# Performance work log

Hardware: AMD Instinct MI355X
Metric: run time of the kernel (lower is better)

## Reference

```python
import jax, jax.numpy as jnp
import numpy as np

NPG = 128      # nodes per graph = g(4) * e(32), forced by rearrange + cnn1 channels
G, E32 = 4, 32
ALPHA = 1.0    # GCN2Conv(in_channels, 1) -> alpha = 1
BETA = 1.0     # theta=None -> beta = 1


def _gcn_norm(edge_index, edge_weight, n):
    """PyG gcn_norm: add self-loops (w=1), sym-normalize by degree at dst."""
    src, dst = edge_index[0], edge_index[1]
    loop = jnp.arange(n)
    src = jnp.concatenate([src, loop])
    dst = jnp.concatenate([dst, loop])
    w = jnp.concatenate([edge_weight, jnp.ones((n,), edge_weight.dtype)])
    deg = jax.ops.segment_sum(w, dst, num_segments=n)
    dinv = jnp.where(deg > 0, jax.lax.rsqrt(deg), 0.0)
    norm = dinv[src] * w * dinv[dst]
    return src, dst, norm


def _propagate(x, src, dst, norm, n):
    # gather -> weight -> scatter-add (SpMM)
    return jax.ops.segment_sum(x[src] * norm[:, None], dst, num_segments=n)


def setup_inputs() -> dict:
    key = jax.random.key(0)
    ks = jax.random.split(key, 10)
    N, E, C, H, CH = 65536, 524288, 128, 512, 256
    x = jax.random.normal(ks[0], (N, C), jnp.float32)
    edge_index = jax.random.randint(ks[1], (2, E), 0, N, dtype=jnp.int64)
    edge_attr = jax.random.uniform(ks[2], (E,), jnp.float32)
    w1_gcn2 = jax.random.normal(ks[3], (C, C), jnp.float32) / np.float32(np.sqrt(C))
    w_gcn = jax.random.normal(ks[4], (C, H), jnp.float32) / np.float32(np.sqrt(C))
    b_gcn = jnp.zeros((H,), jnp.float32)
    w_cnn1 = jax.random.normal(ks[5], (H, 4 * H), jnp.float32) / np.float32(np.sqrt(4 * H))
    b_cnn1 = jnp.zeros((H,), jnp.float32)
    w_cnn2 = jax.random.normal(ks[6], (CH, H), jnp.float32) / np.float32(np.sqrt(H))
    b_cnn2 = jnp.zeros((CH,), jnp.float32)
    w_lin = jax.random.normal(ks[7], (32 * CH,), jnp.float32) / np.float32(np.sqrt(32 * CH))
    b_lin = jnp.zeros((), jnp.float32)
    return {"x": x, "edge_attr": edge_attr, "w1_gcn2": w1_gcn2, "w_gcn": w_gcn,
            "b_gcn": b_gcn, "w_cnn1": w_cnn1, "b_cnn1": b_cnn1, "w_cnn2": w_cnn2,
            "b_cnn2": b_cnn2, "w_lin": w_lin, "b_lin": b_lin, "edge_index": edge_index}


def reference(x, edge_attr, w1_gcn2, w_gcn, b_gcn, w_cnn1, b_cnn1, w_cnn2, b_cnn2,
              w_lin, b_lin, edge_index):
    n = x.shape[0]
    bs = n // NPG
    src, dst, norm = _gcn_norm(edge_index, edge_attr, n)

    # GCN2Conv(C, layer=1): h = (1-a)*A_hat x + a*x0; out = (1-b)*h + b*(h @ W1)
    h = _propagate(x, src, dst, norm, n)
    h = h * (1.0 - ALPHA) + ALPHA * x
    h = (1.0 - BETA) * h + BETA * (h @ w1_gcn2)

    # GCNConv(C, H): A_hat (h @ W) + b
    h = _propagate(h @ w_gcn, src, dst, norm, n) + b_gcn
    h = jnp.tanh(h)

    f = h.shape[1]  # hidden_channels
    # '(bs g e) f -> bs (g f) e', e=32, g=4
    h = h.reshape(bs, G, E32, f).transpose(0, 1, 3, 2).reshape(bs, G * f, E32)
    # 1x1 convs == per-position linears over channel dim
    h = jax.nn.relu(jnp.einsum('bce,oc->boe', h, w_cnn1) + b_cnn1[None, :, None])
    h = jax.nn.relu(jnp.einsum('bce,oc->boe', h, w_cnn2) + b_cnn2[None, :, None])
    # dropout p=0.5 is identity in eval mode
    h = h.reshape(bs, -1)
    out = h @ w_lin + b_lin
    return jax.nn.sigmoid(out)
```

## Files before the change

### kernel.cpp

```cpp
#include <hip/hip_runtime.h>
#include <hip/hip_bf16.h>

#define N_NODES 65536
#define N_EDGES 524288

typedef __attribute__((ext_vector_type(8))) short bf16x8;
typedef __attribute__((ext_vector_type(4))) float f32x4;

__device__ __forceinline__ float bf2f(unsigned short u) {
    union { unsigned int i; float f; } v;
    v.i = ((unsigned int)u) << 16;
    return v.f;
}
__device__ __forceinline__ unsigned short f2bf(float f) {
    union { float f; unsigned int i; } v;
    v.f = f;
    unsigned int r = v.i + 0x7fff + ((v.i >> 16) & 1);
    return (unsigned short)(r >> 16);
}

__global__ void init_k(int* __restrict__ cnt, float* __restrict__ logits) {
    int i = blockIdx.x * 256 + threadIdx.x;
    cnt[i] = 0;
    if (i < 512) logits[i] = 0.0f;
}
__global__ void cnt_k(const int* __restrict__ dst, int* __restrict__ cnt) {
    int e = blockIdx.x * 256 + threadIdx.x;
    atomicAdd(&cnt[dst[e]], 1);
}

__global__ __launch_bounds__(256) void scan1_k(const int* __restrict__ cnt,
                                               int* __restrict__ rp,
                                               int* __restrict__ bsum) {
    __shared__ int s[256];
    int t = threadIdx.x, g = blockIdx.x * 256 + t;
    int v = cnt[g];
    s[t] = v;
    __syncthreads();
    for (int d = 1; d < 256; d <<= 1) {
        int u = (t >= d) ? s[t - d] : 0;
        __syncthreads();
        s[t] += u;
        __syncthreads();
    }
    rp[g] = s[t] - v;
    if (t == 255) bsum[blockIdx.x] = s[255];
}
__global__ __launch_bounds__(256) void scan2_k(int* __restrict__ bsum,
                                               int* __restrict__ rp) {
    __shared__ int s[256];
    int t = threadIdx.x;
    int v = bsum[t];
    s[t] = v;
    __syncthreads();
    for (int d = 1; d < 256; d <<= 1) {
        int u = (t >= d) ? s[t - d] : 0;
        __syncthreads();
        s[t] += u;
        __syncthreads();
    }
    bsum[t] = s[t] - v;
    if (t == 255) rp[65536] = s[255];
}
__global__ __launch_bounds__(256) void scan3_k(int* __restrict__ rp,
                                               const int* __restrict__ bsum,
                                               int* __restrict__ cursor) {
    int t = threadIdx.x, g = blockIdx.x * 256 + t;
    int r = rp[g] + bsum[blockIdx.x];
    rp[g] = r;
    cursor[g] = r;
}

__global__ void scatter_k(const int* __restrict__ src, const int* __restrict__ dst,
                          const float* __restrict__ w,
                          int* __restrict__ cursor, uint2* __restrict__ ep) {
    int e = blockIdx.x * 256 + threadIdx.x;
    int pos = atomicAdd(&cursor[dst[e]], 1);
    uint2 p;
    p.x = (unsigned int)src[e];
    p.y = __float_as_uint(w[e]);
    ep[pos] = p;
}

__global__ void rowsum_k(const int* __restrict__ rp, const uint2* __restrict__ ep,
                         float* __restrict__ dinv) {
    int n = blockIdx.x * 256 + threadIdx.x;
    int beg = rp[n], end = rp[n + 1];
    float s = 1.0f;
    for (int i = beg; i < end; ++i) s += __uint_as_float(ep[i].y);
    dinv[n] = rsqrtf(s);
}

__global__ void xscale_k(const float* __restrict__ x, const float* __restrict__ dinv,
                         __hip_bfloat16* __restrict__ xbf) {
    int i = (blockIdx.x * 256 + threadIdx.x) * 4;
    float d = dinv[i >> 7];
    float4 v = *(const float4*)(x + i);
    alignas(8) __hip_bfloat16 tmp[4] = {
        __float2bfloat16(d * v.x), __float2bfloat16(d * v.y),
        __float2bfloat16(d * v.z), __float2bfloat16(d * v.w)};
    *(ushort4*)((unsigned short*)xbf + i) = *(const ushort4*)tmp;
}

__global__ void wprep_k(const float* __restrict__ wc1, __hip_bfloat16* __restrict__ wc1bf,
                        const float* __restrict__ wc2, __hip_bfloat16* __restrict__ wc2bf,
                        const float* __restrict__ w1, const float* __restrict__ wg,
                        __hip_bfloat16* __restrict__ WT) {
    int bid = blockIdx.x;
    if (bid < 1152) {
        const float* in;
        __hip_bfloat16* outp;
        int i;
        if (bid < 1024) { in = wc1; outp = wc1bf; i = bid * 1024 + threadIdx.x * 4; }
        else            { in = wc2; outp = wc2bf; i = (bid - 1024) * 1024 + threadIdx.x * 4; }
        float4 v = *(const float4*)(in + i);
        alignas(8) __hip_bfloat16 tmp[4] = {__float2bfloat16(v.x), __float2bfloat16(v.y),
                                            __float2bfloat16(v.z), __float2bfloat16(v.w)};
        *(ushort4*)((unsigned short*)outp + i) = *(const ushort4*)tmp;
    } else {
        int t = (bid - 1152) * 256 + threadIdx.x;
        int f = t >> 7, c = t & 127;
        float s = 0.f;
#pragma unroll 8
        for (int m = 0; m < 128; ++m) s += w1[c * 128 + m] * wg[m * 512 + f];
        WT[t] = __float2bfloat16(s);
    }
}

__global__ __launch_bounds__(256) void gather_k(const int* __restrict__ rp,
                                                const uint2* __restrict__ ep,
                                                const unsigned short* __restrict__ xbf,
                                                const float* __restrict__ dinv,
                                                __hip_bfloat16* __restrict__ ybf) {
    int n = (blockIdx.x * 256 + threadIdx.x) >> 6;
    int lane = threadIdx.x & 63;
    int beg = rp[n], end = rp[n + 1];
    float accx, accy;
    {
        unsigned int u = *(const unsigned int*)(xbf + (size_t)n * 128 + lane * 2);
        accx = bf2f((unsigned short)(u & 0xffff));
        accy = bf2f((unsigned short)(u >> 16));
    }
    int i = beg;
    for (; i + 8 <= end; i += 8) {
        uint2 p[8];
        unsigned int u[8];
#pragma unroll
        for (int k = 0; k < 8; ++k) p[k] = ep[i + k];
#pragma unroll
        for (int k = 0; k < 8; ++k)
            u[k] = *(const unsigned int*)(xbf + (size_t)p[k].x * 128 + lane * 2);
#pragma unroll
        for (int k = 0; k < 8; ++k) {
            float c = __uint_as_float(p[k].y);
            accx += c * bf2f((unsigned short)(u[k] & 0xffff));
            accy += c * bf2f((unsigned short)(u[k] >> 16));
        }
    }
    for (; i + 4 <= end; i += 4) {
        uint2 p[4];
        unsigned int u[4];
#pragma unroll
        for (int k = 0; k < 4; ++k) p[k] = ep[i + k];
#pragma unroll
        for (int k = 0; k < 4; ++k)
            u[k] = *(const unsigned int*)(xbf + (size_t)p[k].x * 128 + lane * 2);
#pragma unroll
        for (int k = 0; k < 4; ++k) {
            float c = __uint_as_float(p[k].y);
            accx += c * bf2f((unsigned short)(u[k] & 0xffff));
            accy += c * bf2f((unsigned short)(u[k] >> 16));
        }
    }
    for (; i < end; ++i) {
        uint2 p = ep[i];
        unsigned int u = *(const unsigned int*)(xbf + (size_t)p.x * 128 + lane * 2);
        float c = __uint_as_float(p.y);
        accx += c * bf2f((unsigned short)(u & 0xffff));
        accy += c * bf2f((unsigned short)(u >> 16));
    }
    float dn = dinv[n];
    accx *= dn;
    accy *= dn;
    alignas(4) __hip_bfloat16 o[2] = {__float2bfloat16(accx), __float2bfloat16(accy)};
    *(unsigned int*)((unsigned short*)ybf + (size_t)n * 128 + lane * 2) =
        *(const unsigned int*)o;
}

__device__ __forceinline__ void gll16(const void* g, void* l) {
    __builtin_amdgcn_global_load_lds(
        (const __attribute__((address_space(1))) void*)g,
        (__attribute__((address_space(3))) void*)l, 16, 0, 0);
}

template <int ACT, int OUT_MODE, int SWIZ_NTX>
__global__ __launch_bounds__(256) void gemm_mfma_k(
    const __hip_bfloat16* __restrict__ A, const __hip_bfloat16* __restrict__ B,
    const float* __restrict__ bias, void* __restrict__ Cout,
    const float* __restrict__ wlin, int M, int N, int K) {
    __shared__ char lds[65536];

    const int tid = threadIdx.x;
    const int lane = tid & 63, wid = tid >> 6;
    int bx, by;
    if (SWIZ_NTX > 0) {
        int orig = blockIdx.x;
        int per = gridDim.x / (8 * SWIZ_NTX);
        int xcd = orig & 7, k = orig >> 3;
        by = xcd * per + k / SWIZ_NTX;
        bx = k % SWIZ_NTX;
    } else {
        bx = blockIdx.x;
        by = blockIdx.y;
    }
    const int bm = by * 128, bn = bx * 128;
    const int wr = wid >> 1, wc = wid & 1;

    const int srow = wid * 16 + (lane >> 2);
    const int skcol = (((lane & 3) ^ ((lane >> 3) & 3))) * 8;
    const __hip_bfloat16* Abase = A + (size_t)(bm + srow) * K + skcol;
    const __hip_bfloat16* Bbase = B + (size_t)(bn + srow) * K + skcol;
    const int ldso = wid * 1024;

    f32x4 acc[4][4] = {};

    const int lrow = lane & 15;
    const int lkb = (((lane >> 4) ^ ((lane >> 1) & 3)) << 4);
    const int nk = K >> 5;

    auto stage = [&](int buf, int kt) {
        char* la = lds + buf * 16384;
        char* lb = la + 8192;
        gll16(Abase + kt * 32,                  la + ldso);
        gll16(Abase + kt * 32 + (size_t)64 * K, la + 4096 + ldso);
        gll16(Bbase + kt * 32,                  lb + ldso);
        gll16(Bbase + kt * 32 + (size_t)64 * K, lb + 4096 + ldso);
    };

    stage(0, 0);
    stage(1, 1);
    stage(2, 2);

    for (int kt = 0; kt < nk; ++kt) {
        int ahead = nk - 1 - kt;
        if (ahead >= 2)      asm volatile("s_waitcnt vmcnt(8)" ::: "memory");
        else if (ahead == 1) asm volatile("s_waitcnt vmcnt(4)" ::: "memory");
        else                 asm volatile("s_waitcnt vmcnt(0)" ::: "memory");
        __builtin_amdgcn_s_barrier();
        asm volatile("" ::: "memory");
        if (kt + 3 < nk) stage((kt + 3) & 3, kt + 3);

        const char* la = lds + (kt & 3) * 16384;
        const char* lb = la + 8192;
        bf16x8 af[4], bfr[4];
#pragma unroll
        for (int i = 0; i < 4; ++i)
            af[i] = *(const bf16x8*)(la + (wr * 64 + i * 16 + lrow) * 64 + lkb);
#pragma unroll
        for (int j = 0; j < 4; ++j)
            bfr[j] = *(const bf16x8*)(lb + (wc * 64 + j * 16 + lrow) * 64 + lkb);
        __builtin_amdgcn_s_setprio(1);
#pragma unroll
        for (int i = 0; i < 4; ++i)
#pragma unroll
            for (int j = 0; j < 4; ++j)
                acc[i][j] = __builtin_amdgcn_mfma_f32_16x16x32_bf16(
                    bfr[j], af[i], acc[i][j], 0, 0, 0);
        __builtin_amdgcn_s_setprio(0);
        asm volatile("" ::: "memory");
    }

    const int l15 = lane & 15, lhi = lane >> 4;

    if (OUT_MODE == 3) {
        float p0 = 0.f, p1 = 0.f;
#pragma unroll
        for (int i = 0; i < 4; ++i) {
            int e = (i & 1) * 16 + l15;
#pragma unroll
            for (int j = 0; j < 4; ++j) {
                int n = bn + wc * 64 + j * 16 + lhi * 4;
                float4 bv = *(const float4*)(bias + n);
#pragma unroll
                for (int r = 0; r < 4; ++r) {
                    float v = fmaxf(acc[i][j][r] + ((const float*)&bv)[r], 0.f);
                    float wl = wlin[(n + r) * 32 + e];
                    if (i < 2) p0 += v * wl; else p1 += v * wl;
                }
            }
        }
#pragma unroll
        for (int off = 32; off > 0; off >>= 1) {
            p0 += __shfl_down(p0, off, 64);
            p1 += __shfl_down(p1, off, 64);
        }
        if (lane == 0) {
            int g = (bm >> 5) + wr * 2;
            atomicAdd(&((float*)Cout)[g], p0);
            atomicAdd(&((float*)Cout)[g + 1], p1);
        }
        return;
    }

#pragma unroll
    for (int i = 0; i < 4; ++i) {
        int m = bm + wr * 64 + i * 16 + l15;
#pragma unroll
        for (int j = 0; j < 4; ++j) {
            int n = bn + wc * 64 + j * 16 + lhi * 4;
            float4 bv = *(const float4*)(bias + n);
            ushort4 o;
#pragma unroll
            for (int r = 0; r < 4; ++r) {
                float v = acc[i][j][r] + ((const float*)&bv)[r];
                if (ACT == 1) v = fmaxf(v, 0.f);
                if (ACT == 2) v = 1.0f - 2.0f / (__expf(2.0f * v) + 1.0f);
                ((unsigned short*)&o)[r] = f2bf(v);
            }
            if (OUT_MODE == 1) {
                *(ushort4*)((unsigned short*)Cout + (size_t)m * N + n) = o;
            } else {
                size_t prow = (size_t)(((m >> 7) << 5) | (m & 31));
                size_t idx = prow * 2048 + (size_t)(((m >> 5) & 3) * 512 + n);
                *(ushort4*)((unsigned short*)Cout + idx) = o;
            }
        }
    }
}

__global__ void sigmoid_k(const float* __restrict__ logits,
                          const float* __restrict__ blin, float* __restrict__ out) {
    int b = blockIdx.x * 256 + threadIdx.x;
    out[b] = 1.0f / (1.0f + expf(-(logits[b] + blin[0])));
}

extern "C" void kernel_launch(void* const* d_in, const int* in_sizes, int n_in,
                              void* d_out, int out_size, void* d_ws, size_t ws_size,
                              hipStream_t stream) {
    const float* x    = (const float*)d_in[0];
    const float* eattr= (const float*)d_in[1];
    const float* w1   = (const float*)d_in[2];
    const float* wg   = (const float*)d_in[3];
    const float* bg   = (const float*)d_in[4];
    const float* wc1  = (const float*)d_in[5];
    const float* bc1  = (const float*)d_in[6];
    const float* wc2  = (const float*)d_in[7];
    const float* bc2  = (const float*)d_in[8];
    const float* wlin = (const float*)d_in[9];
    const float* blin = (const float*)d_in[10];
    const int*   ei   = (const int*)d_in[11];
    const int* esrc = ei;
    const int* edst = ei + N_EDGES;
    float* out = (float*)d_out;

    char* ws = (char*)d_ws;
    float*          dinv   = (float*)(ws + 0);
    int*            cnt    = (int*)(ws + 262144);
    int*            rp     = (int*)(ws + 524288);
    int*            cursor = (int*)(ws + 786688);
    uint2*          ep     = (uint2*)(ws + 1048832);
    __hip_bfloat16* WTbf   = (__hip_bfloat16*)(ws + 5243136);
    __hip_bfloat16* ybf    = (__hip_bfloat16*)(ws + 5374208);
    __hip_bfloat16* V      = (__hip_bfloat16*)(ws + 22151424);
    __hip_bfloat16* act1   = (__hip_bfloat16*)(ws + 89260288);
    __hip_bfloat16* wc1bf  = (__hip_bfloat16*)(ws + 106037504);
    __hip_bfloat16* wc2bf  = (__hip_bfloat16*)(ws + 108134656);
    __hip_bfloat16* xbf    = (__hip_bfloat16*)(ws + 108396800);
    float*          logits = (float*)(ws + 125174016);
    int*            bsum   = (int*)(ws + 125176064);
    if (ws_size < (size_t)125177088) return;

    init_k<<<N_NODES / 256, 256, 0, stream>>>(cnt, logits);

    cnt_k<<<N_EDGES / 256, 256, 0, stream>>>(edst, cnt);

    scan1_k<<<256, 256, 0, stream>>>(cnt, rp, bsum);
    scan2_k<<<1, 256, 0, stream>>>(bsum, rp);
    scan3_k<<<256, 256, 0, stream>>>(rp, bsum, cursor);

    scatter_k<<<N_EDGES / 256, 256, 0, stream>>>(esrc, edst, eattr, cursor, ep);

    rowsum_k<<<N_NODES / 256, 256, 0, stream>>>(rp, ep, dinv);

    wprep_k<<<1408, 256, 0, stream>>>(wc1, wc1bf, wc2, wc2bf, w1, wg, WTbf);
    xscale_k<<<(N_NODES * 128 / 4) / 256, 256, 0, stream>>>(x, dinv, xbf);

    gather_k<<<N_NODES / 4, 256, 0, stream>>>(rp, ep,
                                              (const unsigned short*)xbf, dinv, ybf);

    gemm_mfma_k<2, 2, 0><<<dim3(4, 512), 256, 0, stream>>>(
        ybf, WTbf, bg, V, nullptr, 65536, 512, 128);

    gemm_mfma_k<1, 1, 4><<<512, 256, 0, stream>>>(
        V, wc1bf, bc1, act1, nullptr, 16384, 512, 2048);

    gemm_mfma_k<1, 3, 0><<<dim3(2, 128), 256, 0, stream>>>(
        act1, wc2bf, bc2, logits, wlin, 16384, 256, 512);

    sigmoid_k<<<2, 256, 0, stream>>>(logits, blin, out);
}
```

Baseline: 212.7 us.

## Fuse prep kernels, merge rowsum with x scaling, add 64-row final GEMM

Edge counting and weight conversion, including a new pre-packed MFMA fragment layout for the second conv weight, now run in one prep kernel, which removes separate launches. Row-sum and x scaling are merged into a wave-per-node kernel that reduces edge weights with shuffles, then scales and converts x. The last GEMM with its fused linear epilogue moves to a new 64-row tile kernel that reads B directly from registers in packed form, giving twice as many blocks for better occupancy on a small problem. The trade-offs are added code complexity and hand-tuned vmcnt waits that must match the load counts exactly.

```diff
diff --git a/kernel.cpp b/kernel.cpp
--- a/kernel.cpp
+++ b/kernel.cpp
@@ -24,9 +24,42 @@
     cnt[i] = 0;
     if (i < 512) logits[i] = 0.0f;
 }
-__global__ void cnt_k(const int* __restrict__ dst, int* __restrict__ cnt) {
-    int e = blockIdx.x * 256 + threadIdx.x;
-    atomicAdd(&cnt[dst[e]], 1);
+
+__global__ void prep1_k(const int* __restrict__ dst, int* __restrict__ cnt,
+                        const float* __restrict__ wc1, __hip_bfloat16* __restrict__ wc1bf,
+                        const float* __restrict__ wc2, __hip_bfloat16* __restrict__ wc2pk,
+                        const float* __restrict__ w1, const float* __restrict__ wg,
+                        __hip_bfloat16* __restrict__ WT) {
+    int bid = blockIdx.x;
+    if (bid < 2048) {
+        int e = bid * 256 + threadIdx.x;
+        atomicAdd(&cnt[dst[e]], 1);
+    } else if (bid < 3072) {
+        int i = (bid - 2048) * 1024 + threadIdx.x * 4;
+        float4 v = *(const float4*)(wc1 + i);
+        alignas(8) __hip_bfloat16 tmp[4] = {__float2bfloat16(v.x), __float2bfloat16(v.y),
+                                            __float2bfloat16(v.z), __float2bfloat16(v.w)};
+        *(ushort4*)((unsigned short*)wc1bf + i) = *(const ushort4*)tmp;
+    } else if (bid < 3136) {
+        int t = (bid - 3072) * 256 + threadIdx.x;
+        int l = t & 63, grp = t >> 6;
+        int kt = grp & 15, nb = grp >> 4;
+        int n = nb * 16 + (l & 15);
+        int k0 = kt * 32 + (l >> 4) * 8;
+        const float* src = wc2 + (size_t)n * 512 + k0;
+        alignas(16) __hip_bfloat16 tmp[8];
+#pragma unroll
+        for (int e = 0; e < 8; ++e) tmp[e] = __float2bfloat16(src[e]);
+        *(ushort4*)((unsigned short*)wc2pk + (size_t)t * 8)     = *(const ushort4*)tmp;
+        *(ushort4*)((unsigned short*)wc2pk + (size_t)t * 8 + 4) = *(const ushort4*)(tmp + 4);
+    } else {
+        int t = (bid - 3136) * 256 + threadIdx.x;
+        int f = t >> 7, c = t & 127;
+        float s = 0.f;
+#pragma unroll 8
+        for (int m = 0; m < 128; ++m) s += w1[c * 128 + m] * wg[m * 512 + f];
+        WT[t] = __float2bfloat16(s);
+    }
 }
 
 __global__ __launch_bounds__(256) void scan1_k(const int* __restrict__ cnt,
@@ -82,49 +115,26 @@
     ep[pos] = p;
 }
 
-__global__ void rowsum_k(const int* __restrict__ rp, const uint2* __restrict__ ep,
-                         float* __restrict__ dinv) {
-    int n = blockIdx.x * 256 + threadIdx.x;
+__global__ __launch_bounds__(256) void rx_k(const int* __restrict__ rp,
+                                            const uint2* __restrict__ ep,
+                                            const float* __restrict__ x,
+                                            float* __restrict__ dinv,
+                                            __hip_bfloat16* __restrict__ xbf) {
+    int n = (blockIdx.x * 256 + threadIdx.x) >> 6;
+    int lane = threadIdx.x & 63;
     int beg = rp[n], end = rp[n + 1];
-    float s = 1.0f;
-    for (int i = beg; i < end; ++i) s += __uint_as_float(ep[i].y);
-    dinv[n] = rsqrtf(s);
-}
-
-__global__ void xscale_k(const float* __restrict__ x, const float* __restrict__ dinv,
-                         __hip_bfloat16* __restrict__ xbf) {
-    int i = (blockIdx.x * 256 + threadIdx.x) * 4;
-    float d = dinv[i >> 7];
-    float4 v = *(const float4*)(x + i);
-    alignas(8) __hip_bfloat16 tmp[4] = {
-        __float2bfloat16(d * v.x), __float2bfloat16(d * v.y),
-        __float2bfloat16(d * v.z), __float2bfloat16(d * v.w)};
-    *(ushort4*)((unsigned short*)xbf + i) = *(const ushort4*)tmp;
-}
-
-__global__ void wprep_k(const float* __restrict__ wc1, __hip_bfloat16* __restrict__ wc1bf,
-                        const float* __restrict__ wc2, __hip_bfloat16* __restrict__ wc2bf,
-                        const float* __restrict__ w1, const float* __restrict__ wg,
-                        __hip_bfloat16* __restrict__ WT) {
-    int bid = blockIdx.x;
-    if (bid < 1152) {
-        const float* in;
-        __hip_bfloat16* outp;
-        int i;
-        if (bid < 1024) { in = wc1; outp = wc1bf; i = bid * 1024 + threadIdx.x * 4; }
-        else            { in = wc2; outp = wc2bf; i = (bid - 1024) * 1024 + threadIdx.x * 4; }
-        float4 v = *(const float4*)(in + i);
-        alignas(8) __hip_bfloat16 tmp[4] = {__float2bfloat16(v.x), __float2bfloat16(v.y),
-                                            __float2bfloat16(v.z), __float2bfloat16(v.w)};
-        *(ushort4*)((unsigned short*)outp + i) = *(const ushort4*)tmp;
-    } else {
-        int t = (bid - 1152) * 256 + threadIdx.x;
-        int f = t >> 7, c = t & 127;
-        float s = 0.f;
-#pragma unroll 8
-        for (int m = 0; m < 128; ++m) s += w1[c * 128 + m] * wg[m * 512 + f];
-        WT[t] = __float2bfloat16(s);
-    }
+    float s = 0.f;
+    for (int i = beg + lane; i < end; i += 64)
+        s += __uint_as_float(ep[i].y);
+#pragma unroll
+    for (int off = 32; off > 0; off >>= 1) s += __shfl_xor(s, off, 64);
+    float d = rsqrtf(s + 1.0f);
+    if (lane == 0) dinv[n] = d;
+    float2 v = *(const float2*)(x + (size_t)n * 128 + lane * 2);
+    alignas(4) __hip_bfloat16 o[2] = {__float2bfloat16(d * v.x),
+                                      __float2bfloat16(d * v.y)};
+    *(unsigned int*)((unsigned short*)xbf + (size_t)n * 128 + lane * 2) =
+        *(const unsigned int*)o;
 }
 
 __global__ __launch_bounds__(256) void gather_k(const int* __restrict__ rp,
@@ -271,36 +281,6 @@
     }
 
     const int l15 = lane & 15, lhi = lane >> 4;
-
-    if (OUT_MODE == 3) {
-        float p0 = 0.f, p1 = 0.f;
-#pragma unroll
-        for (int i = 0; i < 4; ++i) {
-            int e = (i & 1) * 16 + l15;
-#pragma unroll
-            for (int j = 0; j < 4; ++j) {
-                int n = bn + wc * 64 + j * 16 + lhi * 4;
-                float4 bv = *(const float4*)(bias + n);
-#pragma unroll
-                for (int r = 0; r < 4; ++r) {
-                    float v = fmaxf(acc[i][j][r] + ((const float*)&bv)[r], 0.f);
-                    float wl = wlin[(n + r) * 32 + e];
-                    if (i < 2) p0 += v * wl; else p1 += v * wl;
-                }
-            }
-        }
-#pragma unroll
-        for (int off = 32; off > 0; off >>= 1) {
-            p0 += __shfl_down(p0, off, 64);
-            p1 += __shfl_down(p1, off, 64);
-        }
-        if (lane == 0) {
-            int g = (bm >> 5) + wr * 2;
-            atomicAdd(&((float*)Cout)[g], p0);
-            atomicAdd(&((float*)Cout)[g + 1], p1);
-        }
-        return;
-    }
 
 #pragma unroll
     for (int i = 0; i < 4; ++i) {
@@ -325,6 +305,116 @@
                 *(ushort4*)((unsigned short*)Cout + idx) = o;
             }
         }
+    }
+}
+
+template <int SWIZ_NTX>
+__global__ __launch_bounds__(256) void gemm64_fin_k(
+    const __hip_bfloat16* __restrict__ A, const __hip_bfloat16* __restrict__ Bpk,
+    const float* __restrict__ bias, float* __restrict__ logits,
+    const float* __restrict__ wlin, int M, int N, int K) {
+    __shared__ char lds[16384];
+
+    const int tid = threadIdx.x;
+    const int lane = tid & 63, wid = tid >> 6;
+    const int bx = blockIdx.x, by = blockIdx.y;
+    const int bm = by * 64, bn = bx * 128;
+    const int nk = K >> 5;
+
+    const int srow = wid * 16 + (lane >> 2);
+    const int skcol = (((lane & 3) ^ ((lane >> 3) & 3))) * 8;
+    const __hip_bfloat16* Abase = A + (size_t)(bm + srow) * K + skcol;
+    const int ldso = wid * 1024;
+
+    const __hip_bfloat16* Bp[2];
+#pragma unroll
+    for (int j = 0; j < 2; ++j)
+        Bp[j] = Bpk + ((size_t)((bn >> 4) + wid * 2 + j) * nk) * 512 + lane * 8;
+
+    f32x4 acc[4][2] = {};
+    const int lrow = lane & 15;
+    const int lkb = (((lane >> 4) ^ ((lane >> 1) & 3)) << 4);
+
+    auto stageA = [&](int buf, int kt) {
+        gll16(Abase + kt * 32, lds + buf * 4096 + ldso);
+    };
+
+    bf16x8 b0[2], b1[2];
+    stageA(0, 0);
+    stageA(1, 1);
+    asm volatile("" ::: "memory");
+#pragma unroll
+    for (int j = 0; j < 2; ++j) b0[j] = *(const bf16x8*)(Bp[j]);
+
+#define GEMM_HALF64(KT, BREG)                                                   \
+    {                                                                           \
+        const char* la = lds + ((KT) & 3) * 4096;                               \
+        bf16x8 af[4];                                                           \
+        _Pragma("unroll")                                                       \
+        for (int i = 0; i < 4; ++i)                                             \
+            af[i] = *(const bf16x8*)(la + (i * 16 + lrow) * 64 + lkb);          \
+        __builtin_amdgcn_s_setprio(1);                                          \
+        _Pragma("unroll")                                                       \
+        for (int i = 0; i < 4; ++i)                                             \
+            _Pragma("unroll")                                                   \
+            for (int j = 0; j < 2; ++j)                                         \
+                acc[i][j] = __builtin_amdgcn_mfma_f32_16x16x32_bf16(            \
+                    BREG[j], af[i], acc[i][j], 0, 0, 0);                        \
+        __builtin_amdgcn_s_setprio(0);                                          \
+        asm volatile("" ::: "memory");                                          \
+    }
+
+    for (int kt = 0; kt < nk; kt += 2) {
+        if (kt + 2 < nk) stageA((kt + 2) & 3, kt + 2);
+#pragma unroll
+        for (int j = 0; j < 2; ++j)
+            b1[j] = *(const bf16x8*)(Bp[j] + (size_t)(kt + 1) * 512);
+        if (kt + 2 < nk) asm volatile("s_waitcnt vmcnt(4)" ::: "memory");
+        else             asm volatile("s_waitcnt vmcnt(3)" ::: "memory");
+        __builtin_amdgcn_s_barrier();
+        asm volatile("" ::: "memory");
+        GEMM_HALF64(kt, b0);
+
+        if (kt + 3 < nk) stageA((kt + 3) & 3, kt + 3);
+        if (kt + 2 < nk) {
+#pragma unroll
+            for (int j = 0; j < 2; ++j)
+                b0[j] = *(const bf16x8*)(Bp[j] + (size_t)(kt + 2) * 512);
+        }
+        if (kt + 3 < nk) asm volatile("s_waitcnt vmcnt(4)" ::: "memory");
+        else             asm volatile("s_waitcnt vmcnt(0)" ::: "memory");
+        __builtin_amdgcn_s_barrier();
+        asm volatile("" ::: "memory");
+        GEMM_HALF64(kt + 1, b1);
+    }
+#undef GEMM_HALF64
+
+    const int l15 = lane & 15, lhi = lane >> 4;
+    float p0 = 0.f, p1 = 0.f;
+#pragma unroll
+    for (int i = 0; i < 4; ++i) {
+        int e = (i & 1) * 16 + l15;
+#pragma unroll
+        for (int j = 0; j < 2; ++j) {
+            int n = bn + wid * 32 + j * 16 + lhi * 4;
+            float4 bv = *(const float4*)(bias + n);
+#pragma unroll
+            for (int r = 0; r < 4; ++r) {
+                float v = fmaxf(acc[i][j][r] + ((const float*)&bv)[r], 0.f);
+                float wl = wlin[(n + r) * 32 + e];
+                if (i < 2) p0 += v * wl; else p1 += v * wl;
+            }
+        }
+    }
+#pragma unroll
+    for (int off = 32; off > 0; off >>= 1) {
+        p0 += __shfl_down(p0, off, 64);
+        p1 += __shfl_down(p1, off, 64);
+    }
+    if (lane == 0) {
+        int g = (bm >> 5);
+        atomicAdd(&logits[g], p0);
+        atomicAdd(&logits[g + 1], p1);
     }
 }
 
@@ -364,7 +454,7 @@
     __hip_bfloat16* V      = (__hip_bfloat16*)(ws + 22151424);
     __hip_bfloat16* act1   = (__hip_bfloat16*)(ws + 89260288);
     __hip_bfloat16* wc1bf  = (__hip_bfloat16*)(ws + 106037504);
-    __hip_bfloat16* wc2bf  = (__hip_bfloat16*)(ws + 108134656);
+    __hip_bfloat16* wc2pk  = (__hip_bfloat16*)(ws + 108134656);
     __hip_bfloat16* xbf    = (__hip_bfloat16*)(ws + 108396800);
     float*          logits = (float*)(ws + 125174016);
     int*            bsum   = (int*)(ws + 125176064);
@@ -372,7 +462,8 @@
 
     init_k<<<N_NODES / 256, 256, 0, stream>>>(cnt, logits);
 
-    cnt_k<<<N_EDGES / 256, 256, 0, stream>>>(edst, cnt);
+    prep1_k<<<3392, 256, 0, stream>>>(edst, cnt, wc1, wc1bf, wc2, wc2pk,
+                                      w1, wg, WTbf);
 
     scan1_k<<<256, 256, 0, stream>>>(cnt, rp, bsum);
     scan2_k<<<1, 256, 0, stream>>>(bsum, rp);
@@ -380,10 +471,7 @@
 
     scatter_k<<<N_EDGES / 256, 256, 0, stream>>>(esrc, edst, eattr, cursor, ep);
 
-    rowsum_k<<<N_NODES / 256, 256, 0, stream>>>(rp, ep, dinv);
-
-    wprep_k<<<1408, 256, 0, stream>>>(wc1, wc1bf, wc2, wc2bf, w1, wg, WTbf);
-    xscale_k<<<(N_NODES * 128 / 4) / 256, 256, 0, stream>>>(x, dinv, xbf);
+    rx_k<<<N_NODES / 4, 256, 0, stream>>>(rp, ep, x, dinv, xbf);
 
     gather_k<<<N_NODES / 4, 256, 0, stream>>>(rp, ep,
                                               (const unsigned short*)xbf, dinv, ybf);
@@ -394,8 +482,8 @@
     gemm_mfma_k<1, 1, 4><<<512, 256, 0, stream>>>(
         V, wc1bf, bc1, act1, nullptr, 16384, 512, 2048);
 
-    gemm_mfma_k<1, 3, 0><<<dim3(2, 128), 256, 0, stream>>>(
-        act1, wc2bf, bc2, logits, wlin, 16384, 256, 512);
+    gemm64_fin_k<0><<<dim3(2, 256), 256, 0, stream>>>(
+        act1, wc2pk, bc2, logits, wlin, 16384, 256, 512);
 
     sigmoid_k<<<2, 256, 0, stream>>>(logits, blin, out);
 }
```

Measured after the change: 216.0 us. Within noise of the previous version (+1.5%).
